# Performance work log

Measured on AMD Instinct MI355X. Metric: run time of the kernel, lower is better.

## Reference

```python
import jax, jax.numpy as jnp
import numpy as np

H = 100          # hidden size (hard-coded in module)
B, C, T = 256, 9, 1024
NC = 6           # num_classes


def _lstm_layer(xs, W_ih, W_hh, b, h0, c0):
    """xs: [B,T,In] -> hidden sequence [B,T,H]. Torch gate order i,f,g,o."""
    # Precompute the input projection for all timesteps in one big GEMM.
    pre = jnp.einsum('bti,gi->btg', xs, W_ih) + b   # [B,T,4H]
    pre_t = jnp.swapaxes(pre, 0, 1)                 # [T,B,4H]

    def step(carry, p):
        h, c = carry
        g = p + h @ W_hh.T                          # [B,4H]
        i, f, gg, o = jnp.split(g, 4, axis=-1)
        c = jax.nn.sigmoid(f) * c + jax.nn.sigmoid(i) * jnp.tanh(gg)
        h = jax.nn.sigmoid(o) * jnp.tanh(c)
        return (h, c), h

    (_, _), hs = jax.lax.scan(step, (h0, c0), pre_t)
    return jnp.swapaxes(hs, 0, 1)                   # [B,T,H]


def setup_inputs() -> dict:
    key = jax.random.key(0)
    ks = jax.random.split(key, 14)
    s = 0.1  # ~ uniform(-1/sqrt(H), 1/sqrt(H)) scale of torch default init
    n = lambda k, shape, sc=s: jax.random.normal(k, shape, dtype=jnp.float32) * sc
    return {
        'x':     jax.random.normal(ks[0], (B, C, T), dtype=jnp.float32),
        'h0_1':  jax.random.normal(ks[1], (B, H), dtype=jnp.float32),
        'c0_1':  jax.random.normal(ks[2], (B, H), dtype=jnp.float32),
        'h0_2':  jax.random.normal(ks[3], (B, H), dtype=jnp.float32),
        'c0_2':  jax.random.normal(ks[4], (B, H), dtype=jnp.float32),
        'W_ih1': n(ks[5], (4 * H, C)),
        'W_hh1': n(ks[6], (4 * H, H)),
        'b1':    n(ks[7], (4 * H,)),   # b_ih + b_hh folded together
        'W_ih2': n(ks[8], (4 * H, H)),
        'W_hh2': n(ks[9], (4 * H, H)),
        'b2':    n(ks[10], (4 * H,)),
        'W_fc':  n(ks[11], (NC, H)),
        'b_fc':  n(ks[12], (NC,)),
    }


def reference(x, h0_1, c0_1, h0_2, c0_2, W_ih1, W_hh1, b1,
              W_ih2, W_hh2, b2, W_fc, b_fc):
    xs = jnp.swapaxes(x, 1, 2)                      # [B,T,C] (x.transpose(1,2))
    h1 = _lstm_layer(xs, W_ih1, W_hh1, b1, h0_1, c0_1)   # [B,T,H]
    h2 = _lstm_layer(h1, W_ih2, W_hh2, b2, h0_2, c0_2)   # [B,T,H]
    out = h2[:, -1, :] @ W_fc.T + b_fc              # [B,NC]
    return out
```

## Files before the change

### kernel.cpp

```cpp
#include <hip/hip_runtime.h>

#define HH   100
#define G4   400
#define BB   256
#define CC   9
#define TT   1024
#define NCLS 6
#define XSTR 13

__device__ __forceinline__ float sigm(float x) {
    return __fdividef(1.0f, 1.0f + __expf(-x));
}
__device__ __forceinline__ float tanh_fast(float x) {
    return 2.0f * sigm(2.0f * x) - 1.0f;
}
__device__ __forceinline__ float bcast(float v, int l) {
    return __int_as_float(__builtin_amdgcn_readlane(__float_as_int(v), l));
}

__global__ __launch_bounds__(896, 1)
void lstm_layer1(const float* __restrict__ x,
                 const float* __restrict__ h0,
                 const float* __restrict__ c0,
                 const float* __restrict__ W_ih,
                 const float* __restrict__ W_hh,
                 const float* __restrict__ bias_g,
                 float* __restrict__ h1out)
{
    const int b    = blockIdx.x;
    const int tid  = threadIdx.x;
    const int lane = tid & 63;

    __shared__ float xT[TT * XSTR + 64];
    __shared__ float hb[128];
    __shared__ float p[2][448];

    const float* xb = x + (size_t)b * CC * TT;
    for (int i = tid; i < CC * TT; i += 896) {
        int c  = i >> 10;
        int tp = i & 1023;
        xT[tp * XSTR + c] = xb[i];
    }
    if (tid < 128) hb[tid] = (tid < HH) ? h0[b * HH + tid] : 0.0f;
    float c_reg = (tid < HH) ? c0[b * HH + tid] : 0.0f;

    const bool half0 = (tid < 448);
    const int  r     = half0 ? tid : (tid - 448);
    const int  row   = (r < G4) ? r : 0;

    float w[55], bg = 0.0f;
    if (half0) {
        #pragma unroll
        for (int j = 0; j < CC; ++j) w[j] = W_ih[row * CC + j];
        #pragma unroll
        for (int j = 0; j < 46; ++j) w[CC + j] = W_hh[row * HH + j];
        bg = bias_g[row];
    } else {
        #pragma unroll
        for (int j = 0; j < 54; ++j) w[j] = W_hh[row * HH + 46 + j];
        w[54] = 0.0f;
    }
    #pragma unroll
    for (int j = 0; j < 55; ++j) asm volatile("" : "+v"(w[j]));

    float* hout = h1out + (size_t)b * TT * HH;
    __syncthreads();

    for (int t = 0; t < TT; ++t) {
        if (half0) {
            float vx = xT[t * XSTR + lane];
            float va = hb[lane];
            asm volatile("" : "+v"(vx), "+v"(va));
            float a0 = bg, a1 = 0.f;
            #pragma unroll
            for (int c = 0; c < CC; ++c) {
                float h_ = bcast(vx, c);
                if (c & 1) a1 += h_ * w[c]; else a0 += h_ * w[c];
            }
            #pragma unroll
            for (int j = 0; j < 46; ++j) {
                float h_ = bcast(va, j);
                if (j & 1) a1 += h_ * w[CC + j]; else a0 += h_ * w[CC + j];
            }
            p[0][tid] = a0 + a1;
        } else {
            float vb = hb[46 + lane];
            asm volatile("" : "+v"(vb));
            float a0 = 0.f, a1 = 0.f;
            #pragma unroll
            for (int j = 0; j < 54; ++j) {
                float h_ = bcast(vb, j);
                if (j & 1) a1 += h_ * w[j]; else a0 += h_ * w[j];
            }
            p[1][tid - 448] = a0 + a1;
        }
        __syncthreads();
        if (tid < HH) {
            float ri = p[0][tid]          + p[1][tid];
            float rf = p[0][tid + HH]     + p[1][tid + HH];
            float rg = p[0][tid + 2 * HH] + p[1][tid + 2 * HH];
            float ro = p[0][tid + 3 * HH] + p[1][tid + 3 * HH];
            float cc = sigm(rf) * c_reg + sigm(ri) * tanh_fast(rg);
            c_reg = cc;
            float hv = sigm(ro) * tanh_fast(cc);
            hb[tid] = hv;
            hout[t * HH + tid] = hv;
        }
        __syncthreads();
    }
}

__global__ __launch_bounds__(960, 1)
void lstm_layer2_fc(const float* __restrict__ h1,
                    const float* __restrict__ h0,
                    const float* __restrict__ c0,
                    const float* __restrict__ W_ih,
                    const float* __restrict__ W_hh,
                    const float* __restrict__ bias_g,
                    const float* __restrict__ W_fc,
                    const float* __restrict__ b_fc,
                    float* __restrict__ out)
{
    const int b    = blockIdx.x;
    const int tid  = threadIdx.x;
    const int lane = tid & 63;

    __shared__ float h1buf[2][128];
    __shared__ float h2b[128];
    __shared__ float p[2][448];

    if (tid < 128) {
        h2b[tid] = (tid < HH) ? h0[b * HH + tid] : 0.0f;
        h1buf[0][tid] = 0.0f;
        h1buf[1][tid] = 0.0f;
    }
    float c_reg = (tid < HH) ? c0[b * HH + tid] : 0.0f;

    const bool comp  = (tid < 896);
    const bool half0 = (tid < 448);
    const int  r     = half0 ? tid : (tid - 448);
    const int  row   = (r < G4) ? r : 0;

    float w[HH], bg = 0.0f;
    {
        const float* wsrc = half0 ? (W_ih + row * HH) : (W_hh + row * HH);
        #pragma unroll
        for (int j = 0; j < HH; ++j) w[j] = wsrc[j];
        if (half0) bg = bias_g[row];
    }
    #pragma unroll
    for (int j = 0; j < HH; ++j) asm volatile("" : "+v"(w[j]));

    const float* h1b = h1 + (size_t)b * TT * HH;
    __syncthreads();

    if (tid >= 896) {
        int i = tid - 896;
        if (i < HH / 4)
            ((float4*)h1buf[0])[i] = ((const float4*)h1b)[i];
    }
    __syncthreads();

    for (int t = 0; t < TT; ++t) {
        const int cur = t & 1;
        if (comp) {
            const float* hsrc = half0 ? h1buf[cur] : h2b;
            float va = hsrc[lane];
            float vb = hsrc[64 + lane];
            asm volatile("" : "+v"(va), "+v"(vb));
            float a0 = bg, a1 = 0.f;
            #pragma unroll
            for (int j = 0; j < 64; ++j) {
                float h_ = bcast(va, j);
                if (j & 1) a1 += h_ * w[j]; else a0 += h_ * w[j];
            }
            #pragma unroll
            for (int j = 0; j < 36; ++j) {
                float h_ = bcast(vb, j);
                if (j & 1) a1 += h_ * w[64 + j]; else a0 += h_ * w[64 + j];
            }
            p[half0 ? 0 : 1][r] = a0 + a1;
        } else if ((t + 1) < TT) {
            int i = tid - 896;
            if (i < HH / 4)
                ((float4*)h1buf[cur ^ 1])[i] =
                    ((const float4*)(h1b + (t + 1) * HH))[i];
        }
        __syncthreads();
        if (tid < HH) {
            float ri = p[0][tid]          + p[1][tid];
            float rf = p[0][tid + HH]     + p[1][tid + HH];
            float rg = p[0][tid + 2 * HH] + p[1][tid + 2 * HH];
            float ro = p[0][tid + 3 * HH] + p[1][tid + 3 * HH];
            float cc = sigm(rf) * c_reg + sigm(ri) * tanh_fast(rg);
            c_reg = cc;
            h2b[tid] = sigm(ro) * tanh_fast(cc);
        }
        __syncthreads();
    }

    if (tid < NCLS) {
        float acc = b_fc[tid];
        #pragma unroll 4
        for (int j = 0; j < HH; ++j) acc += W_fc[tid * HH + j] * h2b[j];
        out[b * NCLS + tid] = acc;
    }
}

extern "C" void kernel_launch(void* const* d_in, const int* in_sizes, int n_in,
                              void* d_out, int out_size, void* d_ws, size_t ws_size,
                              hipStream_t stream) {
    const float* x     = (const float*)d_in[0];
    const float* h0_1  = (const float*)d_in[1];
    const float* c0_1  = (const float*)d_in[2];
    const float* h0_2  = (const float*)d_in[3];
    const float* c0_2  = (const float*)d_in[4];
    const float* W_ih1 = (const float*)d_in[5];
    const float* W_hh1 = (const float*)d_in[6];
    const float* b1    = (const float*)d_in[7];
    const float* W_ih2 = (const float*)d_in[8];
    const float* W_hh2 = (const float*)d_in[9];
    const float* b2    = (const float*)d_in[10];
    const float* W_fc  = (const float*)d_in[11];
    const float* b_fc  = (const float*)d_in[12];
    float* out = (float*)d_out;

    float* h1 = (float*)d_ws;

    lstm_layer1<<<BB, 896, 0, stream>>>(x, h0_1, c0_1, W_ih1, W_hh1, b1, h1);
    lstm_layer2_fc<<<BB, 960, 0, stream>>>(h1, h0_2, c0_2, W_ih2, W_hh2, b2,
                                           W_fc, b_fc, out);
}
```

Measured before the change: 2.509 ms.

## Restructure LSTM layers to one gate row per thread with chunked input projection

Layer 1 drops the two-way split of each gate row across thread halves. Each of 448 threads in a 512-thread block now computes a full gate row, which removes the partial-sum combine. Layer 2 is restructured into chunks of 64 timesteps: the h1 slice is staged in shared memory, the input projection for the whole chunk is computed into a shared buffer without per-step barriers, and only the recurrent matvec plus the cell update runs per step. This is meant to take input-projection work off the per-step synchronised path. In exchange, each thread does twice as many serial FMAs per step, fewer waves are resident, and the weight rows are reloaded from global memory once per chunk.

```diff
diff --git a/kernel.cpp b/kernel.cpp
--- a/kernel.cpp
+++ b/kernel.cpp
@@ -7,6 +7,9 @@
 #define TT   1024
 #define NCLS 6
 #define XSTR 13
+#define CH   64
+#define NCH  (TT/CH)
+#define TSTR 128
 
 __device__ __forceinline__ float sigm(float x) {
     return __fdividef(1.0f, 1.0f + __expf(-x));
@@ -18,7 +21,7 @@
     return __int_as_float(__builtin_amdgcn_readlane(__float_as_int(v), l));
 }
 
-__global__ __launch_bounds__(896, 1)
+__global__ __launch_bounds__(512, 2)
 void lstm_layer1(const float* __restrict__ x,
                  const float* __restrict__ h0,
                  const float* __restrict__ c0,
@@ -33,10 +36,10 @@
 
     __shared__ float xT[TT * XSTR + 64];
     __shared__ float hb[128];
-    __shared__ float p[2][448];
+    __shared__ float gates[448];
 
     const float* xb = x + (size_t)b * CC * TT;
-    for (int i = tid; i < CC * TT; i += 896) {
+    for (int i = tid; i < CC * TT; i += 512) {
         int c  = i >> 10;
         int tp = i & 1023;
         xT[tp * XSTR + c] = xb[i];
@@ -44,33 +47,30 @@
     if (tid < 128) hb[tid] = (tid < HH) ? h0[b * HH + tid] : 0.0f;
     float c_reg = (tid < HH) ? c0[b * HH + tid] : 0.0f;
 
-    const bool half0 = (tid < 448);
-    const int  r     = half0 ? tid : (tid - 448);
-    const int  row   = (r < G4) ? r : 0;
-
-    float w[55], bg = 0.0f;
-    if (half0) {
+    const bool comp = (tid < 448);
+    const int  row  = (tid < G4) ? tid : 0;
+
+    float w[CC + HH], bg = 0.0f;
+    if (comp) {
         #pragma unroll
         for (int j = 0; j < CC; ++j) w[j] = W_ih[row * CC + j];
         #pragma unroll
-        for (int j = 0; j < 46; ++j) w[CC + j] = W_hh[row * HH + j];
+        for (int j = 0; j < HH; ++j) w[CC + j] = W_hh[row * HH + j];
         bg = bias_g[row];
-    } else {
         #pragma unroll
-        for (int j = 0; j < 54; ++j) w[j] = W_hh[row * HH + 46 + j];
-        w[54] = 0.0f;
-    }
-    #pragma unroll
-    for (int j = 0; j < 55; ++j) asm volatile("" : "+v"(w[j]));
-
+        for (int j = 0; j < CC + HH; ++j) asm volatile("" : "+v"(w[j]));
+    }
+    const bool isG = (row >= 2 * HH && row < 3 * HH);
     float* hout = h1out + (size_t)b * TT * HH;
     __syncthreads();
 
+    #pragma unroll 1
     for (int t = 0; t < TT; ++t) {
-        if (half0) {
+        if (comp) {
             float vx = xT[t * XSTR + lane];
             float va = hb[lane];
-            asm volatile("" : "+v"(vx), "+v"(va));
+            float vb = hb[64 + lane];
+            asm volatile("" : "+v"(vx), "+v"(va), "+v"(vb));
             float a0 = bg, a1 = 0.f;
             #pragma unroll
             for (int c = 0; c < CC; ++c) {
@@ -78,28 +78,23 @@
                 if (c & 1) a1 += h_ * w[c]; else a0 += h_ * w[c];
             }
             #pragma unroll
-            for (int j = 0; j < 46; ++j) {
+            for (int j = 0; j < 64; ++j) {
                 float h_ = bcast(va, j);
                 if (j & 1) a1 += h_ * w[CC + j]; else a0 += h_ * w[CC + j];
             }
-            p[0][tid] = a0 + a1;
-        } else {
-            float vb = hb[46 + lane];
-            asm volatile("" : "+v"(vb));
-            float a0 = 0.f, a1 = 0.f;
             #pragma unroll
-            for (int j = 0; j < 54; ++j) {
+            for (int j = 0; j < 36; ++j) {
                 float h_ = bcast(vb, j);
-                if (j & 1) a1 += h_ * w[j]; else a0 += h_ * w[j];
-            }
-            p[1][tid - 448] = a0 + a1;
+                if (j & 1) a1 += h_ * w[CC + 64 + j]; else a0 += h_ * w[CC + 64 + j];
+            }
+            gates[tid] = a0 + a1;
         }
         __syncthreads();
         if (tid < HH) {
-            float ri = p[0][tid]          + p[1][tid];
-            float rf = p[0][tid + HH]     + p[1][tid + HH];
-            float rg = p[0][tid + 2 * HH] + p[1][tid + 2 * HH];
-            float ro = p[0][tid + 3 * HH] + p[1][tid + 3 * HH];
+            float ri = gates[tid];
+            float rf = gates[tid + HH];
+            float rg = gates[tid + 2 * HH];
+            float ro = gates[tid + 3 * HH];
             float cc = sigm(rf) * c_reg + sigm(ri) * tanh_fast(rg);
             c_reg = cc;
             float hv = sigm(ro) * tanh_fast(cc);
@@ -108,9 +103,10 @@
         }
         __syncthreads();
     }
-}
-
-__global__ __launch_bounds__(960, 1)
+    (void)isG;
+}
+
+__global__ __launch_bounds__(512, 2)
 void lstm_layer2_fc(const float* __restrict__ h1,
                     const float* __restrict__ h0,
                     const float* __restrict__ c0,
@@ -125,84 +121,112 @@
     const int tid  = threadIdx.x;
     const int lane = tid & 63;
 
-    __shared__ float h1buf[2][128];
-    __shared__ float h2b[128];
-    __shared__ float p[2][448];
-
-    if (tid < 128) {
-        h2b[tid] = (tid < HH) ? h0[b * HH + tid] : 0.0f;
-        h1buf[0][tid] = 0.0f;
-        h1buf[1][tid] = 0.0f;
-    }
+    __shared__ float tile[CH * TSTR];
+    __shared__ float preS[CH * G4];
+    __shared__ float hb[128];
+
+    if (tid < 128) hb[tid] = (tid < HH) ? h0[b * HH + tid] : 0.0f;
     float c_reg = (tid < HH) ? c0[b * HH + tid] : 0.0f;
 
-    const bool comp  = (tid < 896);
-    const bool half0 = (tid < 448);
-    const int  r     = half0 ? tid : (tid - 448);
-    const int  row   = (r < G4) ? r : 0;
-
-    float w[HH], bg = 0.0f;
-    {
-        const float* wsrc = half0 ? (W_ih + row * HH) : (W_hh + row * HH);
-        #pragma unroll
-        for (int j = 0; j < HH; ++j) w[j] = wsrc[j];
-        if (half0) bg = bias_g[row];
-    }
-    #pragma unroll
-    for (int j = 0; j < HH; ++j) asm volatile("" : "+v"(w[j]));
+    const bool comp = (tid < 448);
+    const int  row  = (tid < G4) ? tid : 0;
+    const float bg  = comp ? bias_g[row] : 0.0f;
 
     const float* h1b = h1 + (size_t)b * TT * HH;
     __syncthreads();
 
-    if (tid >= 896) {
-        int i = tid - 896;
-        if (i < HH / 4)
-            ((float4*)h1buf[0])[i] = ((const float4*)h1b)[i];
-    }
-    __syncthreads();
-
-    for (int t = 0; t < TT; ++t) {
-        const int cur = t & 1;
-        if (comp) {
-            const float* hsrc = half0 ? h1buf[cur] : h2b;
-            float va = hsrc[lane];
-            float vb = hsrc[64 + lane];
-            asm volatile("" : "+v"(va), "+v"(vb));
-            float a0 = bg, a1 = 0.f;
-            #pragma unroll
-            for (int j = 0; j < 64; ++j) {
-                float h_ = bcast(va, j);
-                if (j & 1) a1 += h_ * w[j]; else a0 += h_ * w[j];
-            }
-            #pragma unroll
-            for (int j = 0; j < 36; ++j) {
-                float h_ = bcast(vb, j);
-                if (j & 1) a1 += h_ * w[64 + j]; else a0 += h_ * w[64 + j];
-            }
-            p[half0 ? 0 : 1][r] = a0 + a1;
-        } else if ((t + 1) < TT) {
-            int i = tid - 896;
-            if (i < HH / 4)
-                ((float4*)h1buf[cur ^ 1])[i] =
-                    ((const float4*)(h1b + (t + 1) * HH))[i];
-        }
-        __syncthreads();
-        if (tid < HH) {
-            float ri = p[0][tid]          + p[1][tid];
-            float rf = p[0][tid + HH]     + p[1][tid + HH];
-            float rg = p[0][tid + 2 * HH] + p[1][tid + 2 * HH];
-            float ro = p[0][tid + 3 * HH] + p[1][tid + 3 * HH];
-            float cc = sigm(rf) * c_reg + sigm(ri) * tanh_fast(rg);
-            c_reg = cc;
-            h2b[tid] = sigm(ro) * tanh_fast(cc);
-        }
-        __syncthreads();
+    #pragma unroll 1
+    for (int ch = 0; ch < NCH; ++ch) {
+        const int t0 = ch * CH;
+        for (int i = tid; i < CH * 25; i += 512) {
+            int r = i / 25;
+            int c = i - r * 25;
+            ((float4*)(tile + r * TSTR))[c] =
+                ((const float4*)(h1b + (size_t)(t0 + r) * HH))[c];
+        }
+        __syncthreads();
+
+        {
+            const float* wsrc = W_ih + (size_t)row * HH;
+            asm volatile("" : "+v"(wsrc));
+            if (comp) {
+                float wv[HH];
+                #pragma unroll
+                for (int j = 0; j < HH / 4; ++j)
+                    *(float4*)&wv[4 * j] = ((const float4*)wsrc)[j];
+                #pragma unroll
+                for (int j = 0; j < HH; ++j) asm volatile("" : "+v"(wv[j]));
+                #pragma unroll 1
+                for (int t = 0; t < CH; ++t) {
+                    float va = tile[t * TSTR + lane];
+                    float vb = tile[t * TSTR + 64 + lane];
+                    asm volatile("" : "+v"(va), "+v"(vb));
+                    float a0 = bg, a1 = 0.f;
+                    #pragma unroll
+                    for (int j = 0; j < 64; ++j) {
+                        float h_ = bcast(va, j);
+                        if (j & 1) a1 += h_ * wv[j]; else a0 += h_ * wv[j];
+                    }
+                    #pragma unroll
+                    for (int j = 0; j < 36; ++j) {
+                        float h_ = bcast(vb, j);
+                        if (j & 1) a1 += h_ * wv[64 + j]; else a0 += h_ * wv[64 + j];
+                    }
+                    if (tid < G4) preS[t * G4 + row] = a0 + a1;
+                }
+            }
+        }
+        __syncthreads();
+
+        {
+            const float* wsrc = W_hh + (size_t)row * HH;
+            asm volatile("" : "+v"(wsrc));
+            float wv[HH];
+            if (comp) {
+                #pragma unroll
+                for (int j = 0; j < HH / 4; ++j)
+                    *(float4*)&wv[4 * j] = ((const float4*)wsrc)[j];
+                #pragma unroll
+                for (int j = 0; j < HH; ++j) asm volatile("" : "+v"(wv[j]));
+            }
+            #pragma unroll 1
+            for (int t = 0; t < CH; ++t) {
+                if (comp) {
+                    float va = hb[lane];
+                    float vb = hb[64 + lane];
+                    asm volatile("" : "+v"(va), "+v"(vb));
+                    float a0 = 0.f, a1 = 0.f;
+                    #pragma unroll
+                    for (int j = 0; j < 64; ++j) {
+                        float h_ = bcast(va, j);
+                        if (j & 1) a1 += h_ * wv[j]; else a0 += h_ * wv[j];
+                    }
+                    #pragma unroll
+                    for (int j = 0; j < 36; ++j) {
+                        float h_ = bcast(vb, j);
+                        if (j & 1) a1 += h_ * wv[64 + j]; else a0 += h_ * wv[64 + j];
+                    }
+                    if (tid < G4) preS[t * G4 + row] += a0 + a1;
+                }
+                __syncthreads();
+                if (tid < HH) {
+                    float ri = preS[t * G4 + tid];
+                    float rf = preS[t * G4 + HH + tid];
+                    float rg = preS[t * G4 + 2 * HH + tid];
+                    float ro = preS[t * G4 + 3 * HH + tid];
+                    float cc = sigm(rf) * c_reg + sigm(ri) * tanh_fast(rg);
+                    c_reg = cc;
+                    hb[tid] = sigm(ro) * tanh_fast(cc);
+                }
+                __syncthreads();
+            }
+        }
     }
 
     if (tid < NCLS) {
         float acc = b_fc[tid];
         #pragma unroll 4
-        for (int j = 0; j < HH; ++j) acc += W_fc[tid * HH + j] * h2b[j];
+        for (int j = 0; j < HH; ++j) acc += W_fc[tid * HH + j] * hb[j];
         out[b * NCLS + tid] = acc;
     }
 }
@@ -227,7 +251,7 @@
 
     float* h1 = (float*)d_ws;
 
-    lstm_layer1<<<BB, 896, 0, stream>>>(x, h0_1, c0_1, W_ih1, W_hh1, b1, h1);
-    lstm_layer2_fc<<<BB, 960, 0, stream>>>(h1, h0_2, c0_2, W_ih2, W_hh2, b2,
+    lstm_layer1<<<BB, 512, 0, stream>>>(x, h0_1, c0_1, W_ih1, W_hh1, b1, h1);
+    lstm_layer2_fc<<<BB, 512, 0, stream>>>(h1, h0_2, c0_2, W_ih2, W_hh2, b2,
                                            W_fc, b_fc, out);
 }
```

Result: slower. 2.926 ms (+16.6%).
